# Kernel tuning notes

Hardware: AMD Instinct MI355X
Metric: run time of the kernel (lower is better)

Reference implementation:

```python
import jax, jax.numpy as jnp
jax.config.update("jax_enable_x64", True)
import numpy as np

B, IN_DIM, OUT_DIM = 65536, 256, 256
SCALE = 100.0


def setup_inputs() -> dict:
    key = jax.random.key(0)
    k1, k2, k3 = jax.random.split(key, 3)
    c_x = jax.random.randint(k1, (B, IN_DIM), 0, 200, dtype=jnp.int64)
    weight = jax.random.normal(k2, (OUT_DIM, IN_DIM), dtype=jnp.float32)
    true_bias = jax.random.normal(k3, (OUT_DIM,), dtype=jnp.float32)
    in_scale = jnp.ones((1,), dtype=jnp.float32) * jnp.float32(SCALE)
    return {"c_x": c_x, "weight": weight, "true_bias": true_bias, "in_scale": in_scale}


def scale_round(x, scale):
    # torch.round(x * scale).long()
    return jnp.round(x * scale).astype(jnp.int64)


def reference(c_x, weight, true_bias, in_scale):
    scale = jnp.float32(SCALE)
    s = in_scale[0]
    # quantize weight (done in __init__ in the original) and bias (done per-forward)
    w_q = scale_round(weight, scale)                 # [OUT, IN] int64
    b_q = scale_round(true_bias, s * scale)          # [OUT] int64
    # fhe.matrix_product(W, x.T).T == x @ W.T, then add_matrix_vector adds bias per row
    out = jnp.matmul(c_x, w_q.T) + b_q[None, :]      # [B, OUT] int64
    return out, s * scale
```

## Files before the change

kernel.cpp:

```cpp
#include <hip/hip_runtime.h>

typedef _Float16 half8 __attribute__((ext_vector_type(8)));
typedef _Float16 half4 __attribute__((ext_vector_type(4)));
typedef float floatx4 __attribute__((ext_vector_type(4)));

#define IN_DIM 256
#define OUT_DIM 256
#define M_TILE 64
#define ROWSTR 264

__global__ void quant_kernel(const float* __restrict__ w,
                             const float* __restrict__ bias,
                             const float* __restrict__ in_scale,
                             _Float16* __restrict__ wqp,
                             float* __restrict__ bq,
                             float* __restrict__ out_scalar) {
    int t = blockIdx.x * blockDim.x + threadIdx.x;
    if (t < (OUT_DIM * IN_DIM) / 8) {
        int lane = t & 63;
        int ks   = (t >> 6) & 7;
        int ct   = t >> 9;
        int row  = ct * 16 + (lane & 15);
        int k0   = ks * 32 + (lane >> 4) * 8;
        const float* src = w + row * IN_DIM + k0;
        half8 h;
#pragma unroll
        for (int e = 0; e < 8; ++e)
            h[e] = (_Float16)rintf(src[e] * 100.0f);
        *((half8*)wqp + t) = h;
    }
    if (t < OUT_DIM) {
        float s2 = in_scale[0] * 100.0f;
        bq[t] = rintf(bias[t] * s2);
    }
    if (t == 0 && out_scalar != nullptr)
        out_scalar[0] = in_scale[0] * 100.0f;
}

__global__ __launch_bounds__(256, 4) void gemm_kernel(const int* __restrict__ cx,
                                                      const _Float16* __restrict__ wqp,
                                                      const float* __restrict__ bq,
                                                      float* __restrict__ out) {
    __shared__ _Float16 cT[M_TILE * ROWSTR];

    const int t = threadIdx.x;
    const size_t m0 = (size_t)blockIdx.x * M_TILE;

    const int* cbase = cx + m0 * IN_DIM;
#pragma unroll
    for (int i = 0; i < 16; ++i) {
        int flat = i * 1024 + t * 4;
        int4 v = *(const int4*)(cbase + flat);
        int row = flat >> 8;
        int col = flat & 255;
        half4 h;
        h.x = (_Float16)v.x; h.y = (_Float16)v.y;
        h.z = (_Float16)v.z; h.w = (_Float16)v.w;
        *(half4*)&cT[row * ROWSTR + col] = h;
    }
    __syncthreads();

    const int wave = t >> 6;
    const int lane = t & 63;
    const int m16  = lane & 15;
    const int quad = lane >> 4;

    floatx4 acc[4][4] = {};

    const half8* wbase = (const half8*)wqp;
#pragma unroll
    for (int ks = 0; ks < 8; ++ks) {
        half8 afr[4], bfr[4];
#pragma unroll
        for (int i = 0; i < 4; ++i)
            afr[i] = wbase[((wave * 4 + i) * 8 + ks) * 64 + lane];
        const int kb = ks * 32 + quad * 8;
#pragma unroll
        for (int j = 0; j < 4; ++j)
            bfr[j] = *(const half8*)&cT[(j * 16 + m16) * ROWSTR + kb];
#pragma unroll
        for (int i = 0; i < 4; ++i)
#pragma unroll
            for (int j = 0; j < 4; ++j)
                acc[i][j] = __builtin_amdgcn_mfma_f32_16x16x32_f16(afr[i], bfr[j], acc[i][j], 0, 0, 0);
    }

#pragma unroll
    for (int i = 0; i < 4; ++i) {
        int col = wave * 64 + i * 16 + quad * 4;
        floatx4 bv = *(const floatx4*)(bq + col);
#pragma unroll
        for (int j = 0; j < 4; ++j) {
            size_t row = m0 + j * 16 + m16;
            floatx4 v = acc[i][j] + bv;
            *(floatx4*)(out + row * OUT_DIM + col) = v;
        }
    }
}

extern "C" void kernel_launch(void* const* d_in, const int* in_sizes, int n_in,
                              void* d_out, int out_size, void* d_ws, size_t ws_size,
                              hipStream_t stream) {
    const int*   cx       = (const int*)d_in[0];
    const float* w        = (const float*)d_in[1];
    const float* bias     = (const float*)d_in[2];
    const float* in_scale = (const float*)d_in[3];
    float* out = (float*)d_out;

    _Float16* wqp = (_Float16*)d_ws;
    float*    bq  = (float*)((char*)d_ws + OUT_DIM * IN_DIM * 2);

    const int rows = in_sizes[0] / IN_DIM;
    const size_t gemm_elems = (size_t)rows * OUT_DIM;
    float* out_scalar = ((size_t)out_size > gemm_elems) ? (out + gemm_elems) : nullptr;

    quant_kernel<<<32, 256, 0, stream>>>(w, bias, in_scale, wqp, bq, out_scalar);
    gemm_kernel<<<rows / M_TILE, 256, 0, stream>>>(cx, wqp, bq, out);
}
```

Before: 123.4 us.

## Load activation fragments directly from global memory, drop LDS staging

Removes the shared-memory staging of the int activation tile and the block barrier. Each wave now loads and converts its own B fragments straight from global memory. All four waves in a block load the same activation rows, so global/L2 traffic per block rises about fourfold in exchange for no LDS writes and no sync. Output stores become nontemporal to avoid polluting the cache.

New measurement: 155.0 us. +25.6%, slower.

```diff
diff --git a/kernel.cpp b/kernel.cpp
--- a/kernel.cpp
+++ b/kernel.cpp
@@ -1,13 +1,11 @@
 #include <hip/hip_runtime.h>
 
 typedef _Float16 half8 __attribute__((ext_vector_type(8)));
-typedef _Float16 half4 __attribute__((ext_vector_type(4)));
 typedef float floatx4 __attribute__((ext_vector_type(4)));
 
 #define IN_DIM 256
 #define OUT_DIM 256
 #define M_TILE 64
-#define ROWSTR 264
 
 __global__ void quant_kernel(const float* __restrict__ w,
                              const float* __restrict__ bias,
@@ -41,48 +39,44 @@
                                                       const _Float16* __restrict__ wqp,
                                                       const float* __restrict__ bq,
                                                       float* __restrict__ out) {
-    __shared__ _Float16 cT[M_TILE * ROWSTR];
-
-    const int t = threadIdx.x;
-    const size_t m0 = (size_t)blockIdx.x * M_TILE;
-
-    const int* cbase = cx + m0 * IN_DIM;
-#pragma unroll
-    for (int i = 0; i < 16; ++i) {
-        int flat = i * 1024 + t * 4;
-        int4 v = *(const int4*)(cbase + flat);
-        int row = flat >> 8;
-        int col = flat & 255;
-        half4 h;
-        h.x = (_Float16)v.x; h.y = (_Float16)v.y;
-        h.z = (_Float16)v.z; h.w = (_Float16)v.w;
-        *(half4*)&cT[row * ROWSTR + col] = h;
-    }
-    __syncthreads();
-
+    const int t    = threadIdx.x;
     const int wave = t >> 6;
     const int lane = t & 63;
     const int m16  = lane & 15;
     const int quad = lane >> 4;
+    const size_t m0 = (size_t)blockIdx.x * M_TILE;
 
     floatx4 acc[4][4] = {};
 
     const half8* wbase = (const half8*)wqp;
+    const int* crow = cx + (m0 + m16) * IN_DIM + quad * 8;
+
 #pragma unroll
     for (int ks = 0; ks < 8; ++ks) {
-        half8 afr[4], bfr[4];
+        half8 afr[4];
 #pragma unroll
         for (int i = 0; i < 4; ++i)
             afr[i] = wbase[((wave * 4 + i) * 8 + ks) * 64 + lane];
-        const int kb = ks * 32 + quad * 8;
+
+        half8 bfrg[4];
 #pragma unroll
-        for (int j = 0; j < 4; ++j)
-            bfr[j] = *(const half8*)&cT[(j * 16 + m16) * ROWSTR + kb];
+        for (int j = 0; j < 4; ++j) {
+            const int* p = crow + j * 16 * IN_DIM + ks * 32;
+            int4 v0 = *(const int4*)p;
+            int4 v1 = *(const int4*)(p + 4);
+            half8 h;
+            h[0] = (_Float16)(short)v0.x; h[1] = (_Float16)(short)v0.y;
+            h[2] = (_Float16)(short)v0.z; h[3] = (_Float16)(short)v0.w;
+            h[4] = (_Float16)(short)v1.x; h[5] = (_Float16)(short)v1.y;
+            h[6] = (_Float16)(short)v1.z; h[7] = (_Float16)(short)v1.w;
+            bfrg[j] = h;
+        }
+
 #pragma unroll
         for (int i = 0; i < 4; ++i)
 #pragma unroll
             for (int j = 0; j < 4; ++j)
-                acc[i][j] = __builtin_amdgcn_mfma_f32_16x16x32_f16(afr[i], bfr[j], acc[i][j], 0, 0, 0);
+                acc[i][j] = __builtin_amdgcn_mfma_f32_16x16x32_f16(afr[i], bfrg[j], acc[i][j], 0, 0, 0);
     }
 
 #pragma unroll
@@ -93,7 +87,7 @@
         for (int j = 0; j < 4; ++j) {
             size_t row = m0 + j * 16 + m16;
             floatx4 v = acc[i][j] + bv;
-            *(floatx4*)(out + row * OUT_DIM + col) = v;
+            __builtin_nontemporal_store(v, (floatx4*)(out + row * OUT_DIM + col));
         }
     }
 }
```

## Process two row tiles per block, prefetching the second during first compute

Applied to the files above, without the earlier changes.

Each block now handles two 64-row tiles. It loads the second tile's int data into registers while the first tile's MFMA work runs, then converts that data into a second LDS buffer. The aim is to hide global-load latency behind compute and to halve the block count. In exchange, LDS use doubles, the 16 int4 prefetch registers raise register pressure, and launch bounds drop to 2 blocks per SM. The kernel also assumes the tile count is even.

Result: no change. 124.1 us (median of 2 runs) (+0.6%).

```diff
diff --git a/kernel.cpp b/kernel.cpp
--- a/kernel.cpp
+++ b/kernel.cpp
@@ -37,37 +37,10 @@
         out_scalar[0] = in_scale[0] * 100.0f;
 }
 
-__global__ __launch_bounds__(256, 4) void gemm_kernel(const int* __restrict__ cx,
-                                                      const _Float16* __restrict__ wqp,
-                                                      const float* __restrict__ bq,
-                                                      float* __restrict__ out) {
-    __shared__ _Float16 cT[M_TILE * ROWSTR];
-
-    const int t = threadIdx.x;
-    const size_t m0 = (size_t)blockIdx.x * M_TILE;
-
-    const int* cbase = cx + m0 * IN_DIM;
-#pragma unroll
-    for (int i = 0; i < 16; ++i) {
-        int flat = i * 1024 + t * 4;
-        int4 v = *(const int4*)(cbase + flat);
-        int row = flat >> 8;
-        int col = flat & 255;
-        half4 h;
-        h.x = (_Float16)v.x; h.y = (_Float16)v.y;
-        h.z = (_Float16)v.z; h.w = (_Float16)v.w;
-        *(half4*)&cT[row * ROWSTR + col] = h;
-    }
-    __syncthreads();
-
-    const int wave = t >> 6;
-    const int lane = t & 63;
-    const int m16  = lane & 15;
-    const int quad = lane >> 4;
-
-    floatx4 acc[4][4] = {};
-
-    const half8* wbase = (const half8*)wqp;
+__device__ __forceinline__ void compute_tile(const _Float16* __restrict__ cbuf,
+                                             const half8* __restrict__ wbase,
+                                             int wave, int lane, int m16, int quad,
+                                             floatx4 acc[4][4]) {
 #pragma unroll
     for (int ks = 0; ks < 8; ++ks) {
         half8 afr[4], bfr[4];
@@ -77,14 +50,19 @@
         const int kb = ks * 32 + quad * 8;
 #pragma unroll
         for (int j = 0; j < 4; ++j)
-            bfr[j] = *(const half8*)&cT[(j * 16 + m16) * ROWSTR + kb];
+            bfr[j] = *(const half8*)&cbuf[(j * 16 + m16) * ROWSTR + kb];
 #pragma unroll
         for (int i = 0; i < 4; ++i)
 #pragma unroll
             for (int j = 0; j < 4; ++j)
                 acc[i][j] = __builtin_amdgcn_mfma_f32_16x16x32_f16(afr[i], bfr[j], acc[i][j], 0, 0, 0);
     }
+}
 
+__device__ __forceinline__ void store_tile(float* __restrict__ out,
+                                           const float* __restrict__ bq,
+                                           size_t m0, int wave, int m16, int quad,
+                                           floatx4 acc[4][4]) {
 #pragma unroll
     for (int i = 0; i < 4; ++i) {
         int col = wave * 64 + i * 16 + quad * 4;
@@ -96,6 +74,65 @@
             *(floatx4*)(out + row * OUT_DIM + col) = v;
         }
     }
+}
+
+__global__ __launch_bounds__(256, 2) void gemm_kernel(const int* __restrict__ cx,
+                                                      const _Float16* __restrict__ wqp,
+                                                      const float* __restrict__ bq,
+                                                      float* __restrict__ out) {
+    __shared__ _Float16 cT[2][M_TILE * ROWSTR];
+
+    const int t    = threadIdx.x;
+    const int wave = t >> 6;
+    const int lane = t & 63;
+    const int m16  = lane & 15;
+    const int quad = lane >> 4;
+
+    const size_t m0 = (size_t)blockIdx.x * M_TILE;
+    const size_t m1 = m0 + (size_t)gridDim.x * M_TILE;
+    const half8* wbase = (const half8*)wqp;
+
+    {
+        const int* cbase = cx + m0 * IN_DIM;
+#pragma unroll
+        for (int i = 0; i < 16; ++i) {
+            int flat = i * 1024 + t * 4;
+            int4 v = *(const int4*)(cbase + flat);
+            half4 h;
+            h.x = (_Float16)v.x; h.y = (_Float16)v.y;
+            h.z = (_Float16)v.z; h.w = (_Float16)v.w;
+            *(half4*)&cT[0][(flat >> 8) * ROWSTR + (flat & 255)] = h;
+        }
+    }
+    __syncthreads();
+
+    int4 st[16];
+    {
+        const int* cbase = cx + m1 * IN_DIM;
+#pragma unroll
+        for (int i = 0; i < 16; ++i)
+            st[i] = *(const int4*)(cbase + i * 1024 + t * 4);
+    }
+    __builtin_amdgcn_sched_barrier(0);
+
+    floatx4 acc[4][4] = {};
+    compute_tile(cT[0], wbase, wave, lane, m16, quad, acc);
+
+#pragma unroll
+    for (int i = 0; i < 16; ++i) {
+        int flat = i * 1024 + t * 4;
+        half4 h;
+        h.x = (_Float16)st[i].x; h.y = (_Float16)st[i].y;
+        h.z = (_Float16)st[i].z; h.w = (_Float16)st[i].w;
+        *(half4*)&cT[1][(flat >> 8) * ROWSTR + (flat & 255)] = h;
+    }
+    __syncthreads();
+
+    store_tile(out, bq, m0, wave, m16, quad, acc);
+
+    floatx4 acc2[4][4] = {};
+    compute_tile(cT[1], wbase, wave, lane, m16, quad, acc2);
+    store_tile(out, bq, m1, wave, m16, quad, acc2);
 }
 
 extern "C" void kernel_launch(void* const* d_in, const int* in_sizes, int n_in,
@@ -114,6 +151,7 @@
     const size_t gemm_elems = (size_t)rows * OUT_DIM;
     float* out_scalar = ((size_t)out_size > gemm_elems) ? (out + gemm_elems) : nullptr;
 
+    const int ntiles = rows / M_TILE;
     quant_kernel<<<32, 256, 0, stream>>>(w, bias, in_scale, wqp, bq, out_scalar);
-    gemm_kernel<<<rows / M_TILE, 256, 0, stream>>>(cx, wqp, bq, out);
+    gemm_kernel<<<ntiles / 2, 256, 0, stream>>>(cx, wqp, bq, out);
 }
```

## Give each wave its own 16-row slice and drop block-level barrier

Applied to the files above, without the earlier changes.

Each wave now loads and converts its own 16 input rows into a private shared-memory slice and computes all 256 output columns for them in two halves of 8 accumulators. This removes the __syncthreads and the shared-memory reuse of inputs across waves. In exchange every wave streams the whole quantized weight matrix from global/L2 instead of a quarter of it, so weight traffic per block rises fourfold, while accumulator registers drop from 16 to 8 fragments.

Result: slower. 142.4 us (+15.4%).

```diff
diff --git a/kernel.cpp b/kernel.cpp
--- a/kernel.cpp
+++ b/kernel.cpp
@@ -6,7 +6,6 @@
 
 #define IN_DIM 256
 #define OUT_DIM 256
-#define M_TILE 64
 #define ROWSTR 264
 
 __global__ void quant_kernel(const float* __restrict__ w,
@@ -41,59 +40,48 @@
                                                       const _Float16* __restrict__ wqp,
                                                       const float* __restrict__ bq,
                                                       float* __restrict__ out) {
-    __shared__ _Float16 cT[M_TILE * ROWSTR];
+    __shared__ _Float16 cT[4 * 16 * ROWSTR];
 
-    const int t = threadIdx.x;
-    const size_t m0 = (size_t)blockIdx.x * M_TILE;
-
-    const int* cbase = cx + m0 * IN_DIM;
-#pragma unroll
-    for (int i = 0; i < 16; ++i) {
-        int flat = i * 1024 + t * 4;
-        int4 v = *(const int4*)(cbase + flat);
-        int row = flat >> 8;
-        int col = flat & 255;
-        half4 h;
-        h.x = (_Float16)v.x; h.y = (_Float16)v.y;
-        h.z = (_Float16)v.z; h.w = (_Float16)v.w;
-        *(half4*)&cT[row * ROWSTR + col] = h;
-    }
-    __syncthreads();
-
+    const int t    = threadIdx.x;
     const int wave = t >> 6;
     const int lane = t & 63;
     const int m16  = lane & 15;
     const int quad = lane >> 4;
 
-    floatx4 acc[4][4] = {};
+    const size_t r0 = ((size_t)blockIdx.x * 4 + wave) * 16;
+    _Float16* slice = &cT[wave * 16 * ROWSTR];
+
+    const int* cbase = cx + r0 * IN_DIM;
+#pragma unroll
+    for (int i = 0; i < 16; ++i) {
+        int4 v = *(const int4*)(cbase + i * 256 + lane * 4);
+        half4 h;
+        h.x = (_Float16)v.x; h.y = (_Float16)v.y;
+        h.z = (_Float16)v.z; h.w = (_Float16)v.w;
+        *(half4*)&slice[i * ROWSTR + lane * 4] = h;
+    }
 
     const half8* wbase = (const half8*)wqp;
-#pragma unroll
-    for (int ks = 0; ks < 8; ++ks) {
-        half8 afr[4], bfr[4];
-#pragma unroll
-        for (int i = 0; i < 4; ++i)
-            afr[i] = wbase[((wave * 4 + i) * 8 + ks) * 64 + lane];
-        const int kb = ks * 32 + quad * 8;
-#pragma unroll
-        for (int j = 0; j < 4; ++j)
-            bfr[j] = *(const half8*)&cT[(j * 16 + m16) * ROWSTR + kb];
-#pragma unroll
-        for (int i = 0; i < 4; ++i)
-#pragma unroll
-            for (int j = 0; j < 4; ++j)
-                acc[i][j] = __builtin_amdgcn_mfma_f32_16x16x32_f16(afr[i], bfr[j], acc[i][j], 0, 0, 0);
-    }
 
 #pragma unroll
-    for (int i = 0; i < 4; ++i) {
-        int col = wave * 64 + i * 16 + quad * 4;
-        floatx4 bv = *(const floatx4*)(bq + col);
+    for (int h = 0; h < 2; ++h) {
+        floatx4 acc[8] = {};
 #pragma unroll
-        for (int j = 0; j < 4; ++j) {
-            size_t row = m0 + j * 16 + m16;
-            floatx4 v = acc[i][j] + bv;
-            *(floatx4*)(out + row * OUT_DIM + col) = v;
+        for (int ks = 0; ks < 8; ++ks) {
+            const int kb = ks * 32 + quad * 8;
+            half8 bfr = *(const half8*)&slice[m16 * ROWSTR + kb];
+#pragma unroll
+            for (int i = 0; i < 8; ++i) {
+                half8 afr = wbase[(((h * 8 + i) * 8) + ks) * 64 + lane];
+                acc[i] = __builtin_amdgcn_mfma_f32_16x16x32_f16(afr, bfr, acc[i], 0, 0, 0);
+            }
+        }
+#pragma unroll
+        for (int i = 0; i < 8; ++i) {
+            int col = (h * 8 + i) * 16 + quad * 4;
+            floatx4 bv = *(const floatx4*)(bq + col);
+            floatx4 v = acc[i] + bv;
+            *(floatx4*)(out + (r0 + m16) * OUT_DIM + col) = v;
         }
     }
 }
@@ -115,5 +103,5 @@
     float* out_scalar = ((size_t)out_size > gemm_elems) ? (out + gemm_elems) : nullptr;
 
     quant_kernel<<<32, 256, 0, stream>>>(w, bias, in_scale, wqp, bq, out_scalar);
-    gemm_kernel<<<rows / M_TILE, 256, 0, stream>>>(cx, wqp, bq, out);
+    gemm_kernel<<<rows / 64, 256, 0, stream>>>(cx, wqp, bq, out);
 }
```
